# Kernel tuning notes

Measured on AMD Instinct MI355X. Metric: run time of the kernel, lower is better.

## Reference

```python
import jax, jax.numpy as jnp
import numpy as np

B, H, W, C = 16, 56, 56, 512
P = 7           # partition (window) size
NH, DH = 16, 32 # n_heads, head_dim (NH*DH == C)
EPS = 1e-6      # flax nnx LayerNorm default epsilon

def _rel_index(size):
    coords = np.stack(np.meshgrid(np.arange(size), np.arange(size), indexing='ij')).reshape(2, -1)
    rel = coords[:, :, None] - coords[:, None, :]
    rh = rel[0] + (size - 1)
    rw = rel[1] + (size - 1)
    return jnp.asarray(rh * (2 * size - 1) + rw)  # [P*P, P*P] int

REL_IDX = _rel_index(P)

def setup_inputs() -> dict:
    key = jax.random.key(0)
    ks = jax.random.split(key, 6)
    s = lambda k, shape: jax.random.normal(k, shape, jnp.float32) * 0.02
    return {
        'x': jax.random.normal(ks[0], (B, H, W, C), jnp.float32),
        'ln1_s': jnp.ones((C,), jnp.float32), 'ln1_b': jnp.zeros((C,), jnp.float32),
        'w_qkv': s(ks[1], (C, 3 * C)), 'b_qkv': jnp.zeros((3 * C,), jnp.float32),
        'bias_table': s(ks[2], ((2 * P - 1) ** 2, NH)),
        'w_merge': s(ks[3], (C, C)), 'b_merge': jnp.zeros((C,), jnp.float32),
        'ln2_s': jnp.ones((C,), jnp.float32), 'ln2_b': jnp.zeros((C,), jnp.float32),
        'w1': s(ks[4], (C, 4 * C)), 'b1': jnp.zeros((4 * C,), jnp.float32),
        'w2': s(ks[5], (4 * C, C)), 'b2': jnp.zeros((C,), jnp.float32),
    }

def _ln(x, s, b):
    m = x.mean(-1, keepdims=True)
    v = ((x - m) ** 2).mean(-1, keepdims=True)
    return (x - m) * jax.lax.rsqrt(v + EPS) * s + b

def reference(x, ln1_s, ln1_b, w_qkv, b_qkv, bias_table, w_merge, b_merge,
              ln2_s, ln2_b, w1, b1, w2, b2):
    Bn, Hh, Ww, Cc = x.shape
    HP, WP = Hh // P, Ww // P
    # window partition: [B,H,W,C] -> [B, G=HP*WP, P*P, C]
    xp = x.reshape(Bn, HP, P, WP, P, Cc).transpose(0, 1, 3, 2, 4, 5).reshape(Bn, HP * WP, P * P, Cc)
    # --- attention block (pre-LN) ---
    h = _ln(xp, ln1_s, ln1_b)
    qkv = h @ w_qkv + b_qkv
    q, k, v = jnp.split(qkv, 3, axis=-1)
    heads = lambda t: t.reshape(Bn, HP * WP, P * P, NH, DH).transpose(0, 1, 3, 2, 4)
    q = heads(q)
    k = heads(k) * (Cc ** -0.5)  # module scales by feat_dim**-0.5 (faithful)
    v = heads(v)
    # relative position bias gather: [NH, P*P, P*P]
    bias = bias_table[REL_IDX.reshape(-1)].reshape(P * P, P * P, NH).transpose(2, 0, 1)
    scores = jnp.einsum('bghid,bghjd->bghij', q, k) + bias
    attn = jax.nn.softmax(scores, axis=-1)
    o = jnp.einsum('bghij,bghjd->bghid', attn, v)
    o = o.transpose(0, 1, 3, 2, 4).reshape(Bn, HP * WP, P * P, Cc)
    xp = xp + (o @ w_merge + b_merge)
    # --- MLP block (pre-LN) ---
    m = _ln(xp, ln2_s, ln2_b)
    xp = xp + (jax.nn.gelu(m @ w1 + b1) @ w2 + b2)
    # window departition: [B, G, P*P, C] -> [B, H, W, C]
    return xp.reshape(Bn, HP, WP, P, P, Cc).transpose(0, 1, 3, 2, 4, 5).reshape(Bn, Hh, Ww, Cc)
```

## Files before the change

### kernel.cpp

```cpp
#include <hip/hip_runtime.h>
#include <stdint.h>

typedef unsigned short u16;
typedef u16    u16x8  __attribute__((ext_vector_type(8)));
typedef __bf16 bf16x8 __attribute__((ext_vector_type(8)));
typedef float  f32x4  __attribute__((ext_vector_type(4)));

#define TOKS 50176
#define CD   512

__device__ __forceinline__ float bf2f(u16 u) {
    union { unsigned int i; float f; } c; c.i = ((unsigned int)u) << 16; return c.f;
}
__device__ __forceinline__ u16 f2bf(float f) {
    union { float f; unsigned int i; } c; c.f = f;
    unsigned int x = c.i;
    return (u16)((x + 0x7fffu + ((x >> 16) & 1u)) >> 16);
}
__device__ __forceinline__ float gelu_tanh(float x) {
    float t = 0.7978845608028654f * (x + 0.044715f * x * x * x);
    float e = __expf(2.0f * t);
    float th = 1.0f - 2.0f / (e + 1.0f);
    return 0.5f * x * (1.0f + th);
}

typedef const __attribute__((address_space(1))) unsigned int gas_u32;
typedef __attribute__((address_space(3))) unsigned int las_u32;
__device__ __forceinline__ void gload16(const u16* g, u16* l) {
    __builtin_amdgcn_global_load_lds((gas_u32*)g, (las_u32*)l, 16, 0, 0);
}

__global__ __launch_bounds__(256)
void k_transpose_cast(const float* __restrict__ src, u16* __restrict__ dst,
                      const int K, const int N)
{
    __shared__ float tile[32][33];
    const int tx = threadIdx.x & 31, ty = threadIdx.x >> 5;
    const int n0 = blockIdx.x * 32, k0 = blockIdx.y * 32;
    #pragma unroll
    for (int i = 0; i < 4; ++i) {
        int r = ty + i * 8;
        tile[r][tx] = src[(size_t)(k0 + r) * N + n0 + tx];
    }
    __syncthreads();
    #pragma unroll
    for (int i = 0; i < 4; ++i) {
        int r = ty + i * 8;
        dst[(size_t)(n0 + r) * K + k0 + tx] = f2bf(tile[tx][r]);
    }
}

__global__ __launch_bounds__(256)
void k_layernorm(const float* __restrict__ x, const float* __restrict__ g,
                 const float* __restrict__ bvec, u16* __restrict__ out)
{
    const int l = threadIdx.x & 63;
    const int w = threadIdx.x >> 6;
    const size_t row = (size_t)blockIdx.x * 4 + w;
    const float* xr = x + row * CD + l * 8;
    f32x4 v0 = *(const f32x4*)xr;
    f32x4 v1 = *(const f32x4*)(xr + 4);
    float s = 0.f, sq = 0.f;
    #pragma unroll
    for (int i = 0; i < 4; ++i) { s += v0[i]; sq += v0[i] * v0[i]; }
    #pragma unroll
    for (int i = 0; i < 4; ++i) { s += v1[i]; sq += v1[i] * v1[i]; }
    #pragma unroll
    for (int off = 32; off > 0; off >>= 1) {
        s  += __shfl_xor(s, off);
        sq += __shfl_xor(sq, off);
    }
    const float mean = s * (1.0f / 512.0f);
    const float var  = fmaxf(sq * (1.0f / 512.0f) - mean * mean, 0.0f);
    const float rstd = rsqrtf(var + 1e-6f);
    const int c = l * 8;
    f32x4 g0 = *(const f32x4*)(g + c),    g1 = *(const f32x4*)(g + c + 4);
    f32x4 b0 = *(const f32x4*)(bvec + c), b1 = *(const f32x4*)(bvec + c + 4);
    u16x8 o;
    #pragma unroll
    for (int i = 0; i < 4; ++i) o[i]     = f2bf((v0[i] - mean) * rstd * g0[i] + b0[i]);
    #pragma unroll
    for (int i = 0; i < 4; ++i) o[4 + i] = f2bf((v1[i] - mean) * rstd * g1[i] + b1[i]);
    *(u16x8*)(out + row * CD + c) = o;
}

template<int EPI>
__global__ __launch_bounds__(256)
void k_gemm(const u16* __restrict__ A, const u16* __restrict__ Bt,
            const float* __restrict__ bias, const float* __restrict__ resid,
            u16* __restrict__ outb, float* __restrict__ outf,
            const int N, const int K)
{
    __shared__ u16 As[128 * 32];
    __shared__ u16 Bs[128 * 32];
    const int t  = threadIdx.x;
    const int l  = t & 63;
    const int w  = t >> 6;
    const int wr = w >> 1, wc = w & 1;
    const int m0 = blockIdx.y * 128, n0 = blockIdx.x * 128;
    const int kq = l >> 4;
    const int fr = l & 15;

    const int lam  = t ^ ((t >> 3) & 7);
    const int srow = lam >> 2;
    const int skq  = lam & 3;
    const u16* Asrc0 = A  + (size_t)(m0 + srow) * K      + skq * 8;
    const u16* Asrc1 = A  + (size_t)(m0 + 64 + srow) * K + skq * 8;
    const u16* Bsrc0 = Bt + (size_t)(n0 + srow) * K      + skq * 8;
    const u16* Bsrc1 = Bt + (size_t)(n0 + 64 + srow) * K + skq * 8;
    u16* Adst0 = As + w * 512;
    u16* Adst1 = As + 2048 + w * 512;
    u16* Bdst0 = Bs + w * 512;
    u16* Bdst1 = Bs + 2048 + w * 512;

    int offA[4], offB[4];
    #pragma unroll
    for (int mi = 0; mi < 4; ++mi) {
        int lr = (wr * 64 + mi * 16 + fr) * 4 + kq;
        offA[mi] = (lr ^ ((lr >> 3) & 7)) * 8;
    }
    #pragma unroll
    for (int ni = 0; ni < 4; ++ni) {
        int lr = (wc * 64 + ni * 16 + fr) * 4 + kq;
        offB[ni] = (lr ^ ((lr >> 3) & 7)) * 8;
    }

    f32x4 acc[4][4];
    #pragma unroll
    for (int i = 0; i < 4; ++i)
        #pragma unroll
        for (int j = 0; j < 4; ++j) {
            f32x4 z = {0.f, 0.f, 0.f, 0.f};
            acc[i][j] = z;
        }

    for (int k0 = 0; k0 < K; k0 += 32) {
        __syncthreads();
        gload16(Asrc0 + k0, Adst0);
        gload16(Asrc1 + k0, Adst1);
        gload16(Bsrc0 + k0, Bdst0);
        gload16(Bsrc1 + k0, Bdst1);
        asm volatile("s_waitcnt vmcnt(0)" ::: "memory");
        __syncthreads();
        bf16x8 af[4], bfv[4];
        #pragma unroll
        for (int mi = 0; mi < 4; ++mi) af[mi]  = *(const bf16x8*)&As[offA[mi]];
        #pragma unroll
        for (int ni = 0; ni < 4; ++ni) bfv[ni] = *(const bf16x8*)&Bs[offB[ni]];
        #pragma unroll
        for (int mi = 0; mi < 4; ++mi)
            #pragma unroll
            for (int ni = 0; ni < 4; ++ni)
                acc[mi][ni] = __builtin_amdgcn_mfma_f32_16x16x32_bf16(
                    af[mi], bfv[ni], acc[mi][ni], 0, 0, 0);
    }

    float bv[4];
    #pragma unroll
    for (int ni = 0; ni < 4; ++ni) bv[ni] = bias[n0 + wc * 64 + ni * 16 + fr];

    #pragma unroll
    for (int mi = 0; mi < 4; ++mi) {
        #pragma unroll
        for (int r = 0; r < 4; ++r) {
            const size_t row  = (size_t)(m0 + wr * 64 + mi * 16 + kq * 4 + r);
            const size_t base = row * N + n0 + wc * 64 + fr;
            #pragma unroll
            for (int ni = 0; ni < 4; ++ni) {
                float v = acc[mi][ni][r] + bv[ni];
                if (EPI == 1) v = gelu_tanh(v);
                if (EPI == 2) outf[base + ni * 16] = v + resid[base + ni * 16];
                else          outb[base + ni * 16] = f2bf(v);
            }
        }
    }
}

__global__ __launch_bounds__(64)
void k_attn(const u16* __restrict__ qkv, const float* __restrict__ btab,
            u16* __restrict__ o, const int tok_base)
{
    __shared__ float Ss[64 * 53];
    const int l    = threadIdx.x;
    const int widl = blockIdx.x >> 4;
    const int head = blockIdx.x & 15;
    const int bl   = widl >> 6;
    const int g    = widl & 63;
    const int gh   = g >> 3, gw = g & 7;
    const int tok00 = bl * 3136 + gh * 392 + gw * 7;
    const int pl = (l < 49) ? l : 48;
    const int ph = pl / 7, pw = pl - (pl / 7) * 7;
    const int tokl = tok00 + ph * 56 + pw;

    float q[32];
    {
        const size_t qoff = (size_t)tokl * 1536 + head * 32;
        #pragma unroll
        for (int i = 0; i < 4; ++i) {
            u16x8 u = *(const u16x8*)(qkv + qoff + i * 8);
            #pragma unroll
            for (int j = 0; j < 8; ++j) q[i * 8 + j] = bf2f(u[j]);
        }
    }

    float rowmax = -1e30f;
    {
        int j = 0;
        for (int jh = 0; jh < 7; ++jh) {
            for (int jw = 0; jw < 7; ++jw, ++j) {
                const size_t koff = (size_t)(tok00 + jh * 56 + jw) * 1536 + 512 + head * 32;
                float d0 = 0.f, d1 = 0.f, d2 = 0.f, d3 = 0.f;
                #pragma unroll
                for (int i = 0; i < 4; ++i) {
                    u16x8 u = *(const u16x8*)(qkv + koff + i * 8);
                    d0 += q[i * 8 + 0] * bf2f(u[0]); d0 += q[i * 8 + 1] * bf2f(u[1]);
                    d1 += q[i * 8 + 2] * bf2f(u[2]); d1 += q[i * 8 + 3] * bf2f(u[3]);
                    d2 += q[i * 8 + 4] * bf2f(u[4]); d2 += q[i * 8 + 5] * bf2f(u[5]);
                    d3 += q[i * 8 + 6] * bf2f(u[6]); d3 += q[i * 8 + 7] * bf2f(u[7]);
                }
                const float bias = btab[(size_t)((ph - jh + 6) * 13 + (pw - jw + 6)) * 16 + head];
                const float sc = (d0 + d1 + d2 + d3) * 0.04419417382415922f + bias;
                rowmax = fmaxf(rowmax, sc);
                Ss[l * 53 + j] = sc;
            }
        }
    }

    float sum = 0.f;
    for (int j = 0; j < 49; ++j) {
        float p = __expf(Ss[l * 53 + j] - rowmax);
        sum += p;
        Ss[l * 53 + j] = p;
    }

    float oa[32];
    #pragma unroll
    for (int i = 0; i < 32; ++i) oa[i] = 0.f;
    {
        int j = 0;
        for (int jh = 0; jh < 7; ++jh) {
            for (int jw = 0; jw < 7; ++jw, ++j) {
                const size_t voff = (size_t)(tok00 + jh * 56 + jw) * 1536 + 1024 + head * 32;
                const float p = Ss[l * 53 + j];
                #pragma unroll
                for (int i = 0; i < 4; ++i) {
                    u16x8 u = *(const u16x8*)(qkv + voff + i * 8);
                    #pragma unroll
                    for (int jj = 0; jj < 8; ++jj) oa[i * 8 + jj] += p * bf2f(u[jj]);
                }
            }
        }
    }

    if (l < 49) {
        const float inv = 1.0f / sum;
        const size_t obase = (size_t)(tok_base + tokl) * CD + head * 32;
        #pragma unroll
        for (int i = 0; i < 4; ++i) {
            u16x8 u;
            #pragma unroll
            for (int jj = 0; jj < 8; ++jj) u[jj] = f2bf(oa[i * 8 + jj] * inv);
            *(u16x8*)(o + obase + i * 8) = u;
        }
    }
}

extern "C" void kernel_launch(void* const* d_in, const int* in_sizes, int n_in,
                              void* d_out, int out_size, void* d_ws, size_t ws_size,
                              hipStream_t stream)
{
    (void)in_sizes; (void)n_in; (void)out_size; (void)ws_size;
    const float* x     = (const float*)d_in[0];
    const float* ln1_s = (const float*)d_in[1];
    const float* ln1_b = (const float*)d_in[2];
    const float* w_qkv = (const float*)d_in[3];
    const float* b_qkv = (const float*)d_in[4];
    const float* btab  = (const float*)d_in[5];
    const float* w_mrg = (const float*)d_in[6];
    const float* b_mrg = (const float*)d_in[7];
    const float* ln2_s = (const float*)d_in[8];
    const float* ln2_b = (const float*)d_in[9];
    const float* w1    = (const float*)d_in[10];
    const float* b1    = (const float*)d_in[11];
    const float* w2    = (const float*)d_in[12];
    const float* b2    = (const float*)d_in[13];
    float* out = (float*)d_out;

    u16* wqkvT = (u16*)d_ws;
    u16* wmrgT = wqkvT + (size_t)1536 * 512;
    u16* w1T   = wmrgT + (size_t)512 * 512;
    u16* w2T   = w1T   + (size_t)2048 * 512;
    u16* hbuf  = w2T   + (size_t)512 * 2048;
    u16* mbuf  = hbuf  + (size_t)TOKS * 512;
    float* y1  = (float*)(mbuf + (size_t)TOKS * 512);
    u16* qkvc  = (u16*)(y1 + (size_t)TOKS * 512);
    u16* hidc  = qkvc + (size_t)6272 * 1536;

    dim3 B256(256);

    k_transpose_cast<<<dim3(48, 16), B256, 0, stream>>>(w_qkv, wqkvT, 512, 1536);
    k_transpose_cast<<<dim3(16, 16), B256, 0, stream>>>(w_mrg, wmrgT, 512, 512);
    k_transpose_cast<<<dim3(64, 16), B256, 0, stream>>>(w1,   w1T,   512, 2048);
    k_transpose_cast<<<dim3(16, 64), B256, 0, stream>>>(w2,   w2T,   2048, 512);

    k_layernorm<<<dim3(TOKS / 4), B256, 0, stream>>>(x, ln1_s, ln1_b, hbuf);

    for (int c = 0; c < 8; ++c) {
        const size_t tb = (size_t)c * 6272;
        k_gemm<0><<<dim3(12, 49), B256, 0, stream>>>(
            hbuf + tb * 512, wqkvT, b_qkv, nullptr, qkvc, nullptr, 1536, 512);
        k_attn<<<dim3(128 * 16), dim3(64), 0, stream>>>(qkvc, btab, hbuf, (int)tb);
    }

    k_gemm<2><<<dim3(4, 392), B256, 0, stream>>>(
        hbuf, wmrgT, b_mrg, x, nullptr, y1, 512, 512);

    k_layernorm<<<dim3(TOKS / 4), B256, 0, stream>>>(y1, ln2_s, ln2_b, mbuf);

    for (int c = 0; c < 2; ++c) {
        const size_t rb = (size_t)c * 25088;
        k_gemm<1><<<dim3(16, 196), B256, 0, stream>>>(
            mbuf + rb * 512, w1T, b1, nullptr, hidc, nullptr, 2048, 512);
        k_gemm<2><<<dim3(4, 196), B256, 0, stream>>>(
            hidc, w2T, b2, y1 + rb * 512, nullptr, out + rb * 512, 512, 2048);
    }
}
```

Measured before the change: 1.247 ms.

## Use double-buffered 256x256 GEMM tiles, bf16 residual stream, larger attention chunks

Replaces the 128x128 single-buffered GEMM with a 256x256 tile, 512-thread kernel. It double-buffers shared memory so global loads for the next K step overlap MFMA work, and raises wave priority around the MFMA block. The intermediate residual y1 is now stored in bf16 instead of fp32, which halves its traffic but costs precision, with a new epilogue and a bf16 LayerNorm input path to match. The QKV/attention loop runs in 4 chunks instead of 8, with a larger qkv scratch buffer. The bigger tiles give fewer blocks for the merge GEMM and the N=512 GEMMs.

```diff
diff --git a/kernel.cpp b/kernel.cpp
--- a/kernel.cpp
+++ b/kernel.cpp
@@ -50,21 +50,29 @@
     }
 }
 
+template<int BF>
 __global__ __launch_bounds__(256)
-void k_layernorm(const float* __restrict__ x, const float* __restrict__ g,
+void k_layernorm(const void* __restrict__ xin, const float* __restrict__ g,
                  const float* __restrict__ bvec, u16* __restrict__ out)
 {
     const int l = threadIdx.x & 63;
     const int w = threadIdx.x >> 6;
     const size_t row = (size_t)blockIdx.x * 4 + w;
-    const float* xr = x + row * CD + l * 8;
-    f32x4 v0 = *(const f32x4*)xr;
-    f32x4 v1 = *(const f32x4*)(xr + 4);
+    const int c = l * 8;
+    float v[8];
+    if (BF) {
+        u16x8 u = *(const u16x8*)((const u16*)xin + row * CD + c);
+        #pragma unroll
+        for (int i = 0; i < 8; ++i) v[i] = bf2f(u[i]);
+    } else {
+        f32x4 a0 = *(const f32x4*)((const float*)xin + row * CD + c);
+        f32x4 a1 = *(const f32x4*)((const float*)xin + row * CD + c + 4);
+        #pragma unroll
+        for (int i = 0; i < 4; ++i) { v[i] = a0[i]; v[4 + i] = a1[i]; }
+    }
     float s = 0.f, sq = 0.f;
     #pragma unroll
-    for (int i = 0; i < 4; ++i) { s += v0[i]; sq += v0[i] * v0[i]; }
-    #pragma unroll
-    for (int i = 0; i < 4; ++i) { s += v1[i]; sq += v1[i] * v1[i]; }
+    for (int i = 0; i < 8; ++i) { s += v[i]; sq += v[i] * v[i]; }
     #pragma unroll
     for (int off = 32; off > 0; off >>= 1) {
         s  += __shfl_xor(s, off);
@@ -73,86 +81,98 @@
     const float mean = s * (1.0f / 512.0f);
     const float var  = fmaxf(sq * (1.0f / 512.0f) - mean * mean, 0.0f);
     const float rstd = rsqrtf(var + 1e-6f);
-    const int c = l * 8;
     f32x4 g0 = *(const f32x4*)(g + c),    g1 = *(const f32x4*)(g + c + 4);
     f32x4 b0 = *(const f32x4*)(bvec + c), b1 = *(const f32x4*)(bvec + c + 4);
     u16x8 o;
     #pragma unroll
-    for (int i = 0; i < 4; ++i) o[i]     = f2bf((v0[i] - mean) * rstd * g0[i] + b0[i]);
-    #pragma unroll
-    for (int i = 0; i < 4; ++i) o[4 + i] = f2bf((v1[i] - mean) * rstd * g1[i] + b1[i]);
+    for (int i = 0; i < 4; ++i) o[i]     = f2bf((v[i] - mean) * rstd * g0[i] + b0[i]);
+    #pragma unroll
+    for (int i = 0; i < 4; ++i) o[4 + i] = f2bf((v[4+i] - mean) * rstd * g1[i] + b1[i]);
     *(u16x8*)(out + row * CD + c) = o;
 }
 
 template<int EPI>
-__global__ __launch_bounds__(256)
-void k_gemm(const u16* __restrict__ A, const u16* __restrict__ Bt,
-            const float* __restrict__ bias, const float* __restrict__ resid,
-            u16* __restrict__ outb, float* __restrict__ outf,
-            const int N, const int K)
-{
-    __shared__ u16 As[128 * 32];
-    __shared__ u16 Bs[128 * 32];
+__global__ __launch_bounds__(512, 2)
+void k_gemm256(const u16* __restrict__ A, const u16* __restrict__ Bt,
+               const float* __restrict__ bias,
+               const float* __restrict__ residf, const u16* __restrict__ residb,
+               u16* __restrict__ outb, float* __restrict__ outf,
+               const int N, const int K)
+{
+    __shared__ u16 As[2][8192];
+    __shared__ u16 Bs[2][8192];
     const int t  = threadIdx.x;
     const int l  = t & 63;
     const int w  = t >> 6;
-    const int wr = w >> 1, wc = w & 1;
-    const int m0 = blockIdx.y * 128, n0 = blockIdx.x * 128;
-    const int kq = l >> 4;
-    const int fr = l & 15;
-
-    const int lam  = t ^ ((t >> 3) & 7);
-    const int srow = lam >> 2;
-    const int skq  = lam & 3;
-    const u16* Asrc0 = A  + (size_t)(m0 + srow) * K      + skq * 8;
-    const u16* Asrc1 = A  + (size_t)(m0 + 64 + srow) * K + skq * 8;
-    const u16* Bsrc0 = Bt + (size_t)(n0 + srow) * K      + skq * 8;
-    const u16* Bsrc1 = Bt + (size_t)(n0 + 64 + srow) * K + skq * 8;
-    u16* Adst0 = As + w * 512;
-    u16* Adst1 = As + 2048 + w * 512;
-    u16* Bdst0 = Bs + w * 512;
-    u16* Bdst1 = Bs + 2048 + w * 512;
-
-    int offA[4], offB[4];
-    #pragma unroll
-    for (int mi = 0; mi < 4; ++mi) {
-        int lr = (wr * 64 + mi * 16 + fr) * 4 + kq;
-        offA[mi] = (lr ^ ((lr >> 3) & 7)) * 8;
+    const int wr = w >> 2, wc = w & 3;
+    const int m0 = blockIdx.y * 256, n0 = blockIdx.x * 256;
+    const int kq = l >> 4, fr = l & 15;
+
+    int srow0, scol0, srow1, scol1;
+    {
+        int r0 = t >> 2, s0 = t & 3;
+        srow0 = r0; scol0 = (s0 ^ ((r0 >> 1) & 3)) * 8;
+        int sl = 512 + t;
+        int r1 = sl >> 2, s1 = sl & 3;
+        srow1 = r1; scol1 = (s1 ^ ((r1 >> 1) & 3)) * 8;
+    }
+    const u16* Asrc0 = A  + (size_t)(m0 + srow0) * K + scol0;
+    const u16* Asrc1 = A  + (size_t)(m0 + srow1) * K + scol1;
+    const u16* Bsrc0 = Bt + (size_t)(n0 + srow0) * K + scol0;
+    const u16* Bsrc1 = Bt + (size_t)(n0 + srow1) * K + scol1;
+    const int dst0 = w * 512;
+    const int dst1 = 4096 + w * 512;
+
+    int offA[8], offB[4];
+    #pragma unroll
+    for (int mi = 0; mi < 8; ++mi) {
+        int r = wr * 128 + mi * 16 + fr;
+        offA[mi] = r * 32 + (kq ^ ((r >> 1) & 3)) * 8;
     }
     #pragma unroll
     for (int ni = 0; ni < 4; ++ni) {
-        int lr = (wc * 64 + ni * 16 + fr) * 4 + kq;
-        offB[ni] = (lr ^ ((lr >> 3) & 7)) * 8;
-    }
-
-    f32x4 acc[4][4];
-    #pragma unroll
-    for (int i = 0; i < 4; ++i)
+        int r = wc * 64 + ni * 16 + fr;
+        offB[ni] = r * 32 + (kq ^ ((r >> 1) & 3)) * 8;
+    }
+
+    f32x4 acc[8][4];
+    #pragma unroll
+    for (int i = 0; i < 8; ++i)
         #pragma unroll
         for (int j = 0; j < 4; ++j) {
             f32x4 z = {0.f, 0.f, 0.f, 0.f};
             acc[i][j] = z;
         }
 
-    for (int k0 = 0; k0 < K; k0 += 32) {
-        __syncthreads();
-        gload16(Asrc0 + k0, Adst0);
-        gload16(Asrc1 + k0, Adst1);
-        gload16(Bsrc0 + k0, Bdst0);
-        gload16(Bsrc1 + k0, Bdst1);
-        asm volatile("s_waitcnt vmcnt(0)" ::: "memory");
-        __syncthreads();
-        bf16x8 af[4], bfv[4];
-        #pragma unroll
-        for (int mi = 0; mi < 4; ++mi) af[mi]  = *(const bf16x8*)&As[offA[mi]];
-        #pragma unroll
-        for (int ni = 0; ni < 4; ++ni) bfv[ni] = *(const bf16x8*)&Bs[offB[ni]];
-        #pragma unroll
-        for (int mi = 0; mi < 4; ++mi)
+    const int nt = K >> 5;
+    gload16(Asrc0, &As[0][dst0]); gload16(Asrc1, &As[0][dst1]);
+    gload16(Bsrc0, &Bs[0][dst0]); gload16(Bsrc1, &Bs[0][dst1]);
+    asm volatile("s_waitcnt vmcnt(0)" ::: "memory");
+    __syncthreads();
+
+    for (int tt = 0; tt < nt; ++tt) {
+        const int cur = tt & 1;
+        if (tt + 1 < nt) {
+            const int nxt = cur ^ 1;
+            const int ko  = (tt + 1) << 5;
+            gload16(Asrc0 + ko, &As[nxt][dst0]); gload16(Asrc1 + ko, &As[nxt][dst1]);
+            gload16(Bsrc0 + ko, &Bs[nxt][dst0]); gload16(Bsrc1 + ko, &Bs[nxt][dst1]);
+        }
+        bf16x8 af[8], bfv[4];
+        #pragma unroll
+        for (int mi = 0; mi < 8; ++mi) af[mi]  = *(const bf16x8*)&As[cur][offA[mi]];
+        #pragma unroll
+        for (int ni = 0; ni < 4; ++ni) bfv[ni] = *(const bf16x8*)&Bs[cur][offB[ni]];
+        __builtin_amdgcn_s_setprio(1);
+        #pragma unroll
+        for (int mi = 0; mi < 8; ++mi)
             #pragma unroll
             for (int ni = 0; ni < 4; ++ni)
                 acc[mi][ni] = __builtin_amdgcn_mfma_f32_16x16x32_bf16(
                     af[mi], bfv[ni], acc[mi][ni], 0, 0, 0);
+        __builtin_amdgcn_s_setprio(0);
+        asm volatile("s_waitcnt vmcnt(0)" ::: "memory");
+        __syncthreads();
     }
 
     float bv[4];
@@ -160,17 +180,18 @@
     for (int ni = 0; ni < 4; ++ni) bv[ni] = bias[n0 + wc * 64 + ni * 16 + fr];
 
     #pragma unroll
-    for (int mi = 0; mi < 4; ++mi) {
+    for (int mi = 0; mi < 8; ++mi) {
         #pragma unroll
         for (int r = 0; r < 4; ++r) {
-            const size_t row  = (size_t)(m0 + wr * 64 + mi * 16 + kq * 4 + r);
+            const size_t row  = (size_t)(m0 + wr * 128 + mi * 16 + kq * 4 + r);
             const size_t base = row * N + n0 + wc * 64 + fr;
             #pragma unroll
             for (int ni = 0; ni < 4; ++ni) {
                 float v = acc[mi][ni][r] + bv[ni];
                 if (EPI == 1) v = gelu_tanh(v);
-                if (EPI == 2) outf[base + ni * 16] = v + resid[base + ni * 16];
-                else          outb[base + ni * 16] = f2bf(v);
+                if (EPI == 2) v += residf[base + ni * 16];
+                if (EPI == 3) { v += bf2f(residb[base + ni * 16]); outf[base + ni * 16] = v; }
+                else outb[base + ni * 16] = f2bf(v);
             }
         }
     }
@@ -292,36 +313,36 @@
     u16* w2T   = w1T   + (size_t)2048 * 512;
     u16* hbuf  = w2T   + (size_t)512 * 2048;
     u16* mbuf  = hbuf  + (size_t)TOKS * 512;
-    float* y1  = (float*)(mbuf + (size_t)TOKS * 512);
-    u16* qkvc  = (u16*)(y1 + (size_t)TOKS * 512);
-    u16* hidc  = qkvc + (size_t)6272 * 1536;
-
-    dim3 B256(256);
+    u16* y1    = mbuf  + (size_t)TOKS * 512;
+    u16* qkvc  = y1    + (size_t)TOKS * 512;
+    u16* hidc  = qkvc  + (size_t)12544 * 1536;
+
+    dim3 B256(256), B512(512);
 
     k_transpose_cast<<<dim3(48, 16), B256, 0, stream>>>(w_qkv, wqkvT, 512, 1536);
     k_transpose_cast<<<dim3(16, 16), B256, 0, stream>>>(w_mrg, wmrgT, 512, 512);
     k_transpose_cast<<<dim3(64, 16), B256, 0, stream>>>(w1,   w1T,   512, 2048);
     k_transpose_cast<<<dim3(16, 64), B256, 0, stream>>>(w2,   w2T,   2048, 512);
 
-    k_layernorm<<<dim3(TOKS / 4), B256, 0, stream>>>(x, ln1_s, ln1_b, hbuf);
-
-    for (int c = 0; c < 8; ++c) {
-        const size_t tb = (size_t)c * 6272;
-        k_gemm<0><<<dim3(12, 49), B256, 0, stream>>>(
-            hbuf + tb * 512, wqkvT, b_qkv, nullptr, qkvc, nullptr, 1536, 512);
-        k_attn<<<dim3(128 * 16), dim3(64), 0, stream>>>(qkvc, btab, hbuf, (int)tb);
-    }
-
-    k_gemm<2><<<dim3(4, 392), B256, 0, stream>>>(
-        hbuf, wmrgT, b_mrg, x, nullptr, y1, 512, 512);
-
-    k_layernorm<<<dim3(TOKS / 4), B256, 0, stream>>>(y1, ln2_s, ln2_b, mbuf);
+    k_layernorm<0><<<dim3(TOKS / 4), B256, 0, stream>>>(x, ln1_s, ln1_b, hbuf);
+
+    for (int c = 0; c < 4; ++c) {
+        const size_t tb = (size_t)c * 12544;
+        k_gemm256<0><<<dim3(6, 49), B512, 0, stream>>>(
+            hbuf + tb * 512, wqkvT, b_qkv, nullptr, nullptr, qkvc, nullptr, 1536, 512);
+        k_attn<<<dim3(256 * 16), dim3(64), 0, stream>>>(qkvc, btab, hbuf, (int)tb);
+    }
+
+    k_gemm256<2><<<dim3(2, 196), B512, 0, stream>>>(
+        hbuf, wmrgT, b_mrg, x, nullptr, y1, nullptr, 512, 512);
+
+    k_layernorm<1><<<dim3(TOKS / 4), B256, 0, stream>>>(y1, ln2_s, ln2_b, mbuf);
 
     for (int c = 0; c < 2; ++c) {
         const size_t rb = (size_t)c * 25088;
-        k_gemm<1><<<dim3(16, 196), B256, 0, stream>>>(
-            mbuf + rb * 512, w1T, b1, nullptr, hidc, nullptr, 2048, 512);
-        k_gemm<2><<<dim3(4, 196), B256, 0, stream>>>(
-            hidc, w2T, b2, y1 + rb * 512, nullptr, out + rb * 512, 512, 2048);
-    }
-}
+        k_gemm256<1><<<dim3(8, 98), B512, 0, stream>>>(
+            mbuf + rb * 512, w1T, b1, nullptr, nullptr, hidc, nullptr, 2048, 512);
+        k_gemm256<3><<<dim3(2, 98), B512, 0, stream>>>(
+            hidc, w2T, b2, nullptr, y1 + rb * 512, nullptr, out + rb * 512, 512, 2048);
+    }
+}
```

After: 1.242 ms. Within noise of the previous version (-0.4%).
